# Kernel tuning notes

Hardware: AMD Instinct MI355X
Metric: run time of the kernel (lower is better)

Reference implementation:

```python
import jax, jax.numpy as jnp
import numpy as np

B, N, DIM, H, DH, M = 2, 2048, 1024, 16, 64, 512
INNER = H * DH  # 1024
KV = M + 1 + N  # xl mem + null kv + sequence = 2561


def rotate_half(x):
    x1, x2 = jnp.split(x, 2, axis=-1)
    return jnp.concatenate([-x2, x1], axis=-1)


def apply_rotary_pos_emb(pos, t):
    return t * jnp.cos(pos) + rotate_half(t) * jnp.sin(pos)


def setup_inputs() -> dict:
    key = jax.random.key(0)
    ks = jax.random.split(key, 8)
    return {
        "x": jax.random.normal(ks[0], (B, N, DIM), jnp.float32),
        "rotary_q": jax.random.uniform(ks[1], (N, DH), jnp.float32) * 6.28,
        "rotary_k": jax.random.uniform(ks[2], (KV, DH), jnp.float32) * 6.28,
        "xl_memories": jax.random.normal(ks[3], (2, B, H, M, DH), jnp.float32) * 0.02,
        "Wq": jax.random.normal(ks[4], (DIM, INNER), jnp.float32) * 0.02,
        "Wkv": jax.random.normal(ks[5], (DIM, 2 * INNER), jnp.float32) * 0.02,
        "Wout": jax.random.normal(ks[6], (INNER, INNER), jnp.float32) * 0.02,
        "null_kv": jax.random.normal(ks[7], (2, H, DH), jnp.float32),
    }


def reference(x, rotary_q, rotary_k, xl_memories, Wq, Wkv, Wout, null_kv):
    # QKV projections (no bias, matching keras Dense(use_bias=False))
    q = (x @ Wq).reshape(B, N, H, DH).transpose(0, 2, 1, 3)  # b h n d
    k, v = jnp.split(x @ Wkv, 2, axis=-1)
    k = k.reshape(B, N, H, DH).transpose(0, 2, 1, 3)
    v = v.reshape(B, N, H, DH).transpose(0, 2, 1, 3)

    # prepend learned null key/value (1 token)
    nk = jnp.broadcast_to(null_kv[0][None, :, None, :], (B, H, 1, DH))
    nv = jnp.broadcast_to(null_kv[1][None, :, None, :], (B, H, 1, DH))
    k = jnp.concatenate([nk, k], axis=2)
    v = jnp.concatenate([nv, v], axis=2)

    next_xl_memories = jnp.stack([k, v])  # [2, b, h, 1+n, d]

    # prepend XL memories along key axis
    k = jnp.concatenate([xl_memories[0], k], axis=2)  # b h kv d
    v = jnp.concatenate([xl_memories[1], v], axis=2)

    # inline rotary embedding on q and (full) k
    q = apply_rotary_pos_emb(rotary_q, q)
    k = apply_rotary_pos_emb(rotary_k, k)

    # causal attention with bottom-right aligned mask (mem/null tokens visible)
    scale = DH ** -0.5
    sim = jnp.einsum('bhid,bhjd->bhij', q, k) * scale  # b h n kv
    i = jnp.arange(N)[:, None]
    j = jnp.arange(KV)[None, :]
    causal_ok = j <= (i + (KV - N))
    sim = jnp.where(causal_ok, sim, jnp.finfo(sim.dtype).min)
    attn = jax.nn.softmax(sim, axis=-1)
    out = jnp.einsum('bhij,bhjd->bhid', attn, v)  # b h n d

    out = out.transpose(0, 2, 1, 3).reshape(B, N, INNER)
    return out @ Wout, next_xl_memories
```

## Files before the change

kernel.cpp:

```cpp
#include <hip/hip_runtime.h>


typedef short v8s __attribute__((ext_vector_type(8)));
typedef float v4f __attribute__((ext_vector_type(4)));

__device__ __forceinline__ float bf2f(unsigned short x) {
  return __uint_as_float(((unsigned)x) << 16);
}
__device__ __forceinline__ unsigned short f2bf(float f) {
  unsigned u = __float_as_uint(f);
  u += 0x7FFFu + ((u >> 16) & 1u);
  return (unsigned short)(u >> 16);
}

#if __has_builtin(__builtin_amdgcn_exp2f)
#define EXP2(x) __builtin_amdgcn_exp2f(x)
#else
#define EXP2(x) exp2f(x)
#endif

template <int CTRL>
__device__ __forceinline__ float dppf(float x) {
  return __int_as_float(
      __builtin_amdgcn_update_dpp(0, __float_as_int(x), CTRL, 0xF, 0xF, true));
}
#define DPP_X1 0xB1
#define DPP_X2 0x4E
#define DPP_X7 0x141
#define DPP_XF 0x140

__device__ __forceinline__ float red_sum16(float v) {
  v += dppf<DPP_X1>(v);
  v += dppf<DPP_X2>(v);
  v += dppf<DPP_X7>(v);
  v += dppf<DPP_XF>(v);
  return v;
}

__device__ __forceinline__ void gld_lds16(const void* g, void* l) {
  __builtin_amdgcn_global_load_lds(
      (const __attribute__((address_space(1))) unsigned int*)g,
      (__attribute__((address_space(3))) unsigned int*)l, 16, 0, 0);
}

__global__ __launch_bounds__(256) void cvt_bf16(
    const float* __restrict__ S, unsigned short* __restrict__ D, int n4)
{
  const int i = blockIdx.x * 256 + threadIdx.x;
  if (i < n4) {
    const float4 v = ((const float4*)S)[i];
    ushort4 o;
    o.x = f2bf(v.x); o.y = f2bf(v.y); o.z = f2bf(v.z); o.w = f2bf(v.w);
    ((ushort4*)D)[i] = o;
  }
}

template <typename CT>
__global__ __launch_bounds__(256, 2) void gemm_bf16(
    const unsigned short* __restrict__ A,
    const unsigned short* __restrict__ WT,
    CT* __restrict__ C,
    int K, int ldc)
{
  __shared__ unsigned short As[128 * 64];
  __shared__ unsigned short Bs[128 * 64];
  const int tid  = threadIdx.x;
  const int wave = tid >> 6, lane = tid & 63;
  const int l15  = lane & 15, quad = lane >> 4;
  const int wm   = wave >> 1, wn = wave & 1;
  const int row0 = blockIdx.x * 128, col0 = blockIdx.y * 128;
  const int lrow = lane >> 3;
  const int gsw  = (lane & 7) ^ lrow;

  v4f acc[4][4];
  const v4f vzero = {0.f, 0.f, 0.f, 0.f};
#pragma unroll
  for (int i = 0; i < 4; ++i)
#pragma unroll
    for (int j = 0; j < 4; ++j) acc[i][j] = vzero;

  for (int k0 = 0; k0 < K; k0 += 64) {
    __syncthreads();
#pragma unroll
    for (int ro = 0; ro < 4; ++ro) {
      const int chunk = wave * 4 + ro;
      const int arow  = chunk * 8 + lrow;
      gld_lds16(A  + (size_t)(row0 + arow) * K + k0 + gsw * 8, As + chunk * 512);
      gld_lds16(WT + (size_t)(col0 + arow) * K + k0 + gsw * 8, Bs + chunk * 512);
    }
    __syncthreads();

    v8s af[4][2], bf[4][2];
#pragma unroll
    for (int tm = 0; tm < 4; ++tm) {
      const int r = wm * 64 + tm * 16 + l15;
#pragma unroll
      for (int kk = 0; kk < 2; ++kk) {
        const int slot = (kk * 4 + quad) ^ (r & 7);
        af[tm][kk] = *(const v8s*)(As + r * 64 + slot * 8);
      }
    }
#pragma unroll
    for (int tn = 0; tn < 4; ++tn) {
      const int r = wn * 64 + tn * 16 + l15;
#pragma unroll
      for (int kk = 0; kk < 2; ++kk) {
        const int slot = (kk * 4 + quad) ^ (r & 7);
        bf[tn][kk] = *(const v8s*)(Bs + r * 64 + slot * 8);
      }
    }
#pragma unroll
    for (int kk = 0; kk < 2; ++kk)
#pragma unroll
      for (int tm = 0; tm < 4; ++tm)
#pragma unroll
        for (int tn = 0; tn < 4; ++tn)
          acc[tm][tn] = __builtin_amdgcn_mfma_f32_16x16x32_bf16(
              af[tm][kk], bf[tn][kk], acc[tm][tn], 0, 0, 0);
  }

#pragma unroll
  for (int tm = 0; tm < 4; ++tm)
#pragma unroll
    for (int tn = 0; tn < 4; ++tn)
#pragma unroll
      for (int r = 0; r < 4; ++r) {
        const int row = row0 + wm * 64 + tm * 16 + quad * 4 + r;
        const int col = col0 + wn * 64 + tn * 16 + l15;
        if constexpr (sizeof(CT) == 2)
          C[(size_t)row * ldc + col] = (CT)f2bf(acc[tm][tn][r]);
        else
          C[(size_t)row * ldc + col] = (CT)acc[tm][tn][r];
      }
}

__global__ __launch_bounds__(256) void transpose_wt(
    const float* __restrict__ S0,
    const float* __restrict__ S1,
    int c0, int c1, int K,
    unsigned short* __restrict__ D)
{
  __shared__ float T[64][65];
  const int k0 = blockIdx.x * 64, n0 = blockIdx.y * 64;
  const int tid = threadIdx.x;
#pragma unroll
  for (int ro = 0; ro < 4; ++ro) {
    const int idx = ro * 256 + tid;
    const int kr = idx >> 4, ch = idx & 15;
    const int n = n0 + ch * 4;
    float4 val;
    if (n < c0) val = *(const float4*)(S0 + (size_t)(k0 + kr) * c0 + n);
    else        val = *(const float4*)(S1 + (size_t)(k0 + kr) * c1 + (n - c0));
    T[kr][ch * 4 + 0] = val.x; T[kr][ch * 4 + 1] = val.y;
    T[kr][ch * 4 + 2] = val.z; T[kr][ch * 4 + 3] = val.w;
  }
  __syncthreads();
#pragma unroll
  for (int ro = 0; ro < 2; ++ro) {
    const int idx = ro * 256 + tid;
    const int nl = idx >> 3, ch = idx & 7;
    __align__(16) unsigned short tmp[8];
#pragma unroll
    for (int e = 0; e < 8; ++e) tmp[e] = f2bf(T[ch * 8 + e][nl]);
    *(uint4*)(D + (size_t)(n0 + nl) * K + k0 + ch * 8) = *(const uint4*)tmp;
  }
}

__global__ __launch_bounds__(256) void assemble(
    const unsigned short* __restrict__ QKV,
    const float* __restrict__ rq,
    const float* __restrict__ rk,
    const float* __restrict__ xlm,
    const float* __restrict__ nkv,
    unsigned short* __restrict__ Qrot,
    unsigned short* __restrict__ Kf,
    unsigned short* __restrict__ Vn,
    float* __restrict__ nxl)
{
  const int gw = blockIdx.x * 4 + (threadIdx.x >> 6);
  const int d  = threadIdx.x & 63;
  const int RK = 32 * 2561;
  if (gw < RK) {
    const int bh = gw / 2561;
    const int j  = gw - bh * 2561;
    const int b  = bh >> 4, h = bh & 15;
    float kx, vx;
    if (j < 512) {
      const size_t i0 = (((size_t)(b * 16 + h)) * 512 + j) * 64 + d;
      kx = xlm[i0];
      vx = xlm[1048576 + i0];
    } else if (j == 512) {
      kx = nkv[h * 64 + d];
      vx = nkv[1024 + h * 64 + d];
    } else {
      const size_t rowb = ((size_t)(b * 2048 + (j - 513))) * 3072;
      kx = bf2f(QKV[rowb + 1024 + h * 64 + d]);
      vx = bf2f(QKV[rowb + 2048 + h * 64 + d]);
    }
    Vn[(((size_t)bh) * 2561 + j) * 64 + d] = f2bf(vx);
    if (j >= 512) {
      const size_t o0 = (((size_t)(b * 16 + h)) * 2049 + (j - 512)) * 64 + d;
      nxl[o0] = kx;
      nxl[4196352 + o0] = vx;
    }
    const float ang = rk[j * 64 + d];
    const float cs = __cosf(ang), sn = __sinf(ang);
    const float part = __shfl_xor(kx, 32);
    const float kr = kx * cs + (d < 32 ? -part : part) * sn;
    Kf[(((size_t)bh) * 2624 + j) * 64 + d] = f2bf(kr);
  } else {
    const int g2 = gw - RK;
    const int bh = g2 >> 11, n = g2 & 2047;
    const int b  = bh >> 4, h = bh & 15;
    const float qx = bf2f(QKV[((size_t)(b * 2048 + n)) * 3072 + h * 64 + d]);
    const float ang = rq[n * 64 + d];
    const float cs = __cosf(ang), sn = __sinf(ang);
    const float part = __shfl_xor(qx, 32);
    const float qr = qx * cs + (d < 32 ? -part : part) * sn;
    Qrot[(((size_t)bh) * 2048 + n) * 64 + d] = f2bf(qr * 0.18033688f);
  }
}

__global__ __launch_bounds__(256) void transpose_v(
    const unsigned short* __restrict__ Vn,
    unsigned short* __restrict__ VTp)
{
  __shared__ unsigned short T[64][72];
  const int j0 = blockIdx.x * 64;
  const int bh = blockIdx.y;
  const int tid = threadIdx.x;
#pragma unroll
  for (int ro = 0; ro < 2; ++ro) {
    const int idx = ro * 256 + tid;
    const int jr = idx >> 3, ch = idx & 7;
    uint4 val = make_uint4(0, 0, 0, 0);
    if (j0 + jr < 2561)
      val = *(const uint4*)(Vn + (((size_t)bh) * 2561 + j0 + jr) * 64 + ch * 8);
    *(uint4*)(&T[jr][ch * 8]) = val;
  }
  __syncthreads();
#pragma unroll
  for (int ro = 0; ro < 2; ++ro) {
    const int idx = ro * 256 + tid;
    const int dl = idx >> 3, ch = idx & 7;
    __align__(16) unsigned short tmp[8];
#pragma unroll
    for (int e = 0; e < 8; ++e) tmp[e] = T[ch * 8 + e][dl];
    *(uint4*)(VTp + (((size_t)bh) * 64 + dl) * 2624 + j0 + ch * 8) = *(const uint4*)tmp;
  }
}

__global__ __launch_bounds__(256, 2) void attn_fa(
    const unsigned short* __restrict__ Qr,
    const unsigned short* __restrict__ Kf,
    const unsigned short* __restrict__ VTp,
    unsigned short* __restrict__ Ao)
{
  const int qb = 15 - (int)blockIdx.x;
  const int bh = blockIdx.y;
  const int b = bh >> 4, h = bh & 15;
  __shared__ unsigned short QPs[128 * 72];
  __shared__ unsigned short Ks[64 * 72];
  __shared__ unsigned short Vs[64 * 72];
  const int tid = threadIdx.x;
  const int wave = tid >> 6, lane = tid & 63;
  const int l15 = lane & 15, quad = lane >> 4;
  const v4f vzero = {0.f, 0.f, 0.f, 0.f};

  {
    const unsigned short* Qg = Qr + (((size_t)bh) * 2048 + qb * 128) * 64;
#pragma unroll
    for (int ro = 0; ro < 4; ++ro) {
      const int idx = ro * 256 + tid;
      const int row = idx >> 3, ch = idx & 7;
      *(uint4*)(QPs + row * 72 + ch * 8) = *(const uint4*)(Qg + row * 64 + ch * 8);
    }
  }
  __syncthreads();
  v8s qf[2][2];
#pragma unroll
  for (int mt = 0; mt < 2; ++mt) {
    const int r = mt * 64 + wave * 16 + l15;
    qf[mt][0] = *(const v8s*)(QPs + r * 72 + quad * 8);
    qf[mt][1] = *(const v8s*)(QPs + r * 72 + 32 + quad * 8);
  }
  unsigned short* Pw = QPs + wave * 32 * 72;

  float l_i[2][4] = {{0.f,0.f,0.f,0.f},{0.f,0.f,0.f,0.f}};
  v4f O[2][4];
#pragma unroll
  for (int mt = 0; mt < 2; ++mt)
#pragma unroll
    for (int dt = 0; dt < 4; ++dt) O[mt][dt] = vzero;

  const unsigned short* Kg0 = Kf + (size_t)bh * 2624 * 64;
  const unsigned short* Vg0 = VTp + (size_t)bh * 64 * 2624;
  const int ntiles = (2 * qb + 11 <= 41) ? (2 * qb + 11) : 41;
  const int tfast  = 2 * qb + 7;

  const int srow = tid >> 3, sch = tid & 7;
  const int srow1 = srow + 32;

#define PREFETCH(t, ka, kb, va, vb)                                          \
  {                                                                          \
    const int j0p = (t) * 64;                                                \
    ka = *(const uint4*)(Kg0 + (size_t)(j0p + srow) * 64 + sch * 8);         \
    va = *(const uint4*)(Vg0 + (size_t)srow * 2624 + j0p + sch * 8);         \
    kb = *(const uint4*)(Kg0 + (size_t)(j0p + srow1) * 64 + sch * 8);        \
    vb = *(const uint4*)(Vg0 + (size_t)srow1 * 2624 + j0p + sch * 8);        \
  }
#define STAGE(ka, kb, va, vb)                                                \
  {                                                                          \
    *(uint4*)(Ks + srow * 72 + sch * 8) = ka;                                \
    *(uint4*)(Vs + srow * 72 + sch * 8) = va;                                \
    *(uint4*)(Ks + srow1 * 72 + sch * 8) = kb;                               \
    *(uint4*)(Vs + srow1 * 72 + sch * 8) = vb;                               \
  }

  auto compute_tile = [&](int j0, bool masked) {
    v4f s[2][4];
#pragma unroll
    for (int jt = 0; jt < 4; ++jt) {
      const v8s kfr0 = *(const v8s*)(Ks + (jt * 16 + l15) * 72 + quad * 8);
      const v8s kfr1 = *(const v8s*)(Ks + (jt * 16 + l15) * 72 + 32 + quad * 8);
#pragma unroll
      for (int mt = 0; mt < 2; ++mt) {
        v4f c = vzero;
        c = __builtin_amdgcn_mfma_f32_16x16x32_bf16(qf[mt][0], kfr0, c, 0, 0, 0);
        c = __builtin_amdgcn_mfma_f32_16x16x32_bf16(qf[mt][1], kfr1, c, 0, 0, 0);
        s[mt][jt] = c;
      }
    }

    if (masked) {
#pragma unroll
      for (int mt = 0; mt < 2; ++mt) {
        const int ibase = qb * 128 + mt * 64 + wave * 16 + quad * 4 + 513;
#pragma unroll
        for (int jt = 0; jt < 4; ++jt) {
          const int jg = j0 + jt * 16 + l15;
#pragma unroll
          for (int r = 0; r < 4; ++r)
            s[mt][jt][r] = (jg <= ibase + r) ? s[mt][jt][r] : -1e30f;
        }
      }
    }

#pragma unroll
    for (int mt = 0; mt < 2; ++mt)
#pragma unroll
      for (int r = 0; r < 4; ++r) {
        const float p0 = EXP2(s[mt][0][r]);
        const float p1 = EXP2(s[mt][1][r]);
        const float p2 = EXP2(s[mt][2][r]);
        const float p3 = EXP2(s[mt][3][r]);
        l_i[mt][r] += red_sum16(p0 + p1 + p2 + p3);
        const int prow = (mt * 16 + quad * 4 + r) * 72 + l15;
        Pw[prow]      = f2bf(p0);
        Pw[prow + 16] = f2bf(p1);
        Pw[prow + 32] = f2bf(p2);
        Pw[prow + 48] = f2bf(p3);
      }
    __asm__ volatile("s_waitcnt lgkmcnt(0)" ::: "memory");

    v8s pf[2][2];
#pragma unroll
    for (int mt = 0; mt < 2; ++mt) {
      pf[mt][0] = *(const v8s*)(Pw + (mt * 16 + l15) * 72 + quad * 8);
      pf[mt][1] = *(const v8s*)(Pw + (mt * 16 + l15) * 72 + 32 + quad * 8);
    }
#pragma unroll
    for (int dt = 0; dt < 4; ++dt) {
      const v8s vf0 = *(const v8s*)(Vs + (dt * 16 + l15) * 72 + quad * 8);
      const v8s vf1 = *(const v8s*)(Vs + (dt * 16 + l15) * 72 + 32 + quad * 8);
#pragma unroll
      for (int mt = 0; mt < 2; ++mt) {
        v4f c = O[mt][dt];
        c = __builtin_amdgcn_mfma_f32_16x16x32_bf16(pf[mt][0], vf0, c, 0, 0, 0);
        c = __builtin_amdgcn_mfma_f32_16x16x32_bf16(pf[mt][1], vf1, c, 0, 0, 0);
        O[mt][dt] = c;
      }
    }
  };

  uint4 k0a, k0b, v0a, v0b, k1a, k1b, v1a, v1b;
  PREFETCH(0, k0a, k0b, v0a, v0b);
  for (int t = 0; t < ntiles; t += 2) {
    __syncthreads();
    STAGE(k0a, k0b, v0a, v0b);
    if (t + 1 < ntiles) PREFETCH(t + 1, k1a, k1b, v1a, v1b);
    __syncthreads();
    compute_tile(t * 64, t > tfast);
    if (t + 1 >= ntiles) break;
    __syncthreads();
    STAGE(k1a, k1b, v1a, v1b);
    if (t + 2 < ntiles) PREFETCH(t + 2, k0a, k0b, v0a, v0b);
    __syncthreads();
    compute_tile((t + 1) * 64, (t + 1) > tfast);
  }
#undef PREFETCH
#undef STAGE

#pragma unroll
  for (int mt = 0; mt < 2; ++mt)
#pragma unroll
    for (int r = 0; r < 4; ++r) {
      const float linv = 1.0f / l_i[mt][r];
      const int n = qb * 128 + mt * 64 + wave * 16 + quad * 4 + r;
      const size_t rowbase = ((size_t)b * 2048 + n) * 1024 + h * 64;
#pragma unroll
      for (int dt = 0; dt < 4; ++dt)
        Ao[rowbase + dt * 16 + l15] = f2bf(O[mt][dt][r] * linv);
    }
}

extern "C" void kernel_launch(void* const* d_in, const int* in_sizes, int n_in,
                              void* d_out, int out_size, void* d_ws, size_t ws_size,
                              hipStream_t stream)
{
  const float* x    = (const float*)d_in[0];
  const float* rq   = (const float*)d_in[1];
  const float* rk   = (const float*)d_in[2];
  const float* xlm  = (const float*)d_in[3];
  const float* Wq   = (const float*)d_in[4];
  const float* Wkv  = (const float*)d_in[5];
  const float* Wout = (const float*)d_in[6];
  const float* nkv  = (const float*)d_in[7];
  float* out = (float*)d_out;
  float* nxl = out + 4194304;
  char* ws = (char*)d_ws;
  unsigned short* QKV   = (unsigned short*)(ws + 0);
  unsigned short* xbf   = (unsigned short*)(ws + 25165824);
  unsigned short* Ao    = (unsigned short*)(ws + 25165824);
  unsigned short* WqkvT = (unsigned short*)(ws + 33554432);
  unsigned short* WoutT = (unsigned short*)(ws + 39845888);
  unsigned short* Qrot  = (unsigned short*)(ws + 41943040);
  unsigned short* Kf    = (unsigned short*)(ws + 50331648);
  unsigned short* Vn    = (unsigned short*)(ws + 61079552);
  unsigned short* VTp   = (unsigned short*)(ws + 71569408);

  cvt_bf16<<<4096, 256, 0, stream>>>(x, xbf, 1048576);
  transpose_wt<<<dim3(16, 48), 256, 0, stream>>>(Wq, Wkv, 1024, 2048, 1024, WqkvT);
  transpose_wt<<<dim3(16, 16), 256, 0, stream>>>(Wout, Wout, 1024, 1024, 1024, WoutT);
  gemm_bf16<unsigned short><<<dim3(32, 24), 256, 0, stream>>>(xbf, WqkvT, QKV, 1024, 3072);
  assemble<<<36872, 256, 0, stream>>>(QKV, rq, rk, xlm, nkv, Qrot, Kf, Vn, nxl);
  transpose_v<<<dim3(41, 32), 256, 0, stream>>>(Vn, VTp);
  attn_fa<<<dim3(16, 32), 256, 0, stream>>>(Qrot, Kf, VTp, Ao);
  gemm_bf16<float><<<dim3(32, 8), 256, 0, stream>>>(Ao, WoutT, out, 1024, 1024);
}
```

Measured before the change: 253.4 us.

## Halve attention query tile to 64 rows and stagger block-to-tile mapping

The flash-attention kernel now processes 64 query rows per block instead of 128, with each wave holding one 16-row fragment. This doubles the grid to 1024 blocks and raises the launch-bounds occupancy hint to 4 blocks per CU. The query-block index is rotated by blockIdx.y to interleave long and short causal workloads across the grid. The aim is better load balance and latency hiding, at the cost of loading each K/V tile twice as often per query row, which lowers arithmetic intensity.

```diff
diff --git a/kernel.cpp b/kernel.cpp
--- a/kernel.cpp
+++ b/kernel.cpp
@@ -250,16 +250,16 @@
   }
 }
 
-__global__ __launch_bounds__(256, 2) void attn_fa(
+__global__ __launch_bounds__(256, 4) void attn_fa(
     const unsigned short* __restrict__ Qr,
     const unsigned short* __restrict__ Kf,
     const unsigned short* __restrict__ VTp,
     unsigned short* __restrict__ Ao)
 {
-  const int qb = 15 - (int)blockIdx.x;
   const int bh = blockIdx.y;
+  const int qb = 31 - (int)((blockIdx.x + blockIdx.y) & 31);
   const int b = bh >> 4, h = bh & 15;
-  __shared__ unsigned short QPs[128 * 72];
+  __shared__ unsigned short QPs[64 * 72];
   __shared__ unsigned short Ks[64 * 72];
   __shared__ unsigned short Vs[64 * 72];
   const int tid = threadIdx.x;
@@ -268,35 +268,32 @@
   const v4f vzero = {0.f, 0.f, 0.f, 0.f};
 
   {
-    const unsigned short* Qg = Qr + (((size_t)bh) * 2048 + qb * 128) * 64;
-#pragma unroll
-    for (int ro = 0; ro < 4; ++ro) {
+    const unsigned short* Qg = Qr + (((size_t)bh) * 2048 + qb * 64) * 64;
+#pragma unroll
+    for (int ro = 0; ro < 2; ++ro) {
       const int idx = ro * 256 + tid;
       const int row = idx >> 3, ch = idx & 7;
       *(uint4*)(QPs + row * 72 + ch * 8) = *(const uint4*)(Qg + row * 64 + ch * 8);
     }
   }
   __syncthreads();
-  v8s qf[2][2];
-#pragma unroll
-  for (int mt = 0; mt < 2; ++mt) {
-    const int r = mt * 64 + wave * 16 + l15;
-    qf[mt][0] = *(const v8s*)(QPs + r * 72 + quad * 8);
-    qf[mt][1] = *(const v8s*)(QPs + r * 72 + 32 + quad * 8);
-  }
-  unsigned short* Pw = QPs + wave * 32 * 72;
-
-  float l_i[2][4] = {{0.f,0.f,0.f,0.f},{0.f,0.f,0.f,0.f}};
-  v4f O[2][4];
-#pragma unroll
-  for (int mt = 0; mt < 2; ++mt)
-#pragma unroll
-    for (int dt = 0; dt < 4; ++dt) O[mt][dt] = vzero;
+  v8s qf[2];
+  {
+    const int r = wave * 16 + l15;
+    qf[0] = *(const v8s*)(QPs + r * 72 + quad * 8);
+    qf[1] = *(const v8s*)(QPs + r * 72 + 32 + quad * 8);
+  }
+  unsigned short* Pw = QPs + wave * 16 * 72;
+
+  float l_i[4] = {0.f, 0.f, 0.f, 0.f};
+  v4f O[4];
+#pragma unroll
+  for (int dt = 0; dt < 4; ++dt) O[dt] = vzero;
 
   const unsigned short* Kg0 = Kf + (size_t)bh * 2624 * 64;
   const unsigned short* Vg0 = VTp + (size_t)bh * 64 * 2624;
-  const int ntiles = (2 * qb + 11 <= 41) ? (2 * qb + 11) : 41;
-  const int tfast  = 2 * qb + 7;
+  const int ntiles = (qb + 10 <= 41) ? (qb + 10) : 41;
+  const int tfast  = qb + 7;
 
   const int srow = tid >> 3, sch = tid & 7;
   const int srow1 = srow + 32;
@@ -318,68 +315,54 @@
   }
 
   auto compute_tile = [&](int j0, bool masked) {
-    v4f s[2][4];
+    v4f s[4];
 #pragma unroll
     for (int jt = 0; jt < 4; ++jt) {
       const v8s kfr0 = *(const v8s*)(Ks + (jt * 16 + l15) * 72 + quad * 8);
       const v8s kfr1 = *(const v8s*)(Ks + (jt * 16 + l15) * 72 + 32 + quad * 8);
-#pragma unroll
-      for (int mt = 0; mt < 2; ++mt) {
-        v4f c = vzero;
-        c = __builtin_amdgcn_mfma_f32_16x16x32_bf16(qf[mt][0], kfr0, c, 0, 0, 0);
-        c = __builtin_amdgcn_mfma_f32_16x16x32_bf16(qf[mt][1], kfr1, c, 0, 0, 0);
-        s[mt][jt] = c;
+      v4f c = vzero;
+      c = __builtin_amdgcn_mfma_f32_16x16x32_bf16(qf[0], kfr0, c, 0, 0, 0);
+      c = __builtin_amdgcn_mfma_f32_16x16x32_bf16(qf[1], kfr1, c, 0, 0, 0);
+      s[jt] = c;
+    }
+
+    if (masked) {
+      const int ibase = qb * 64 + wave * 16 + quad * 4 + 513;
+#pragma unroll
+      for (int jt = 0; jt < 4; ++jt) {
+        const int jg = j0 + jt * 16 + l15;
+#pragma unroll
+        for (int r = 0; r < 4; ++r)
+          s[jt][r] = (jg <= ibase + r) ? s[jt][r] : -1e30f;
       }
     }
 
-    if (masked) {
-#pragma unroll
-      for (int mt = 0; mt < 2; ++mt) {
-        const int ibase = qb * 128 + mt * 64 + wave * 16 + quad * 4 + 513;
-#pragma unroll
-        for (int jt = 0; jt < 4; ++jt) {
-          const int jg = j0 + jt * 16 + l15;
-#pragma unroll
-          for (int r = 0; r < 4; ++r)
-            s[mt][jt][r] = (jg <= ibase + r) ? s[mt][jt][r] : -1e30f;
-        }
-      }
-    }
-
-#pragma unroll
-    for (int mt = 0; mt < 2; ++mt)
-#pragma unroll
-      for (int r = 0; r < 4; ++r) {
-        const float p0 = EXP2(s[mt][0][r]);
-        const float p1 = EXP2(s[mt][1][r]);
-        const float p2 = EXP2(s[mt][2][r]);
-        const float p3 = EXP2(s[mt][3][r]);
-        l_i[mt][r] += red_sum16(p0 + p1 + p2 + p3);
-        const int prow = (mt * 16 + quad * 4 + r) * 72 + l15;
-        Pw[prow]      = f2bf(p0);
-        Pw[prow + 16] = f2bf(p1);
-        Pw[prow + 32] = f2bf(p2);
-        Pw[prow + 48] = f2bf(p3);
-      }
+#pragma unroll
+    for (int r = 0; r < 4; ++r) {
+      const float p0 = EXP2(s[0][r]);
+      const float p1 = EXP2(s[1][r]);
+      const float p2 = EXP2(s[2][r]);
+      const float p3 = EXP2(s[3][r]);
+      l_i[r] += red_sum16(p0 + p1 + p2 + p3);
+      const int prow = (quad * 4 + r) * 72 + l15;
+      Pw[prow]      = f2bf(p0);
+      Pw[prow + 16] = f2bf(p1);
+      Pw[prow + 32] = f2bf(p2);
+      Pw[prow + 48] = f2bf(p3);
+    }
     __asm__ volatile("s_waitcnt lgkmcnt(0)" ::: "memory");
 
-    v8s pf[2][2];
-#pragma unroll
-    for (int mt = 0; mt < 2; ++mt) {
-      pf[mt][0] = *(const v8s*)(Pw + (mt * 16 + l15) * 72 + quad * 8);
-      pf[mt][1] = *(const v8s*)(Pw + (mt * 16 + l15) * 72 + 32 + quad * 8);
-    }
+    v8s pf[2];
+    pf[0] = *(const v8s*)(Pw + l15 * 72 + quad * 8);
+    pf[1] = *(const v8s*)(Pw + l15 * 72 + 32 + quad * 8);
 #pragma unroll
     for (int dt = 0; dt < 4; ++dt) {
       const v8s vf0 = *(const v8s*)(Vs + (dt * 16 + l15) * 72 + quad * 8);
       const v8s vf1 = *(const v8s*)(Vs + (dt * 16 + l15) * 72 + 32 + quad * 8);
-#pragma unroll
-      for (int mt = 0; mt < 2; ++mt) {
-        v4f c = O[mt][dt];
-        c = __builtin_amdgcn_mfma_f32_16x16x32_bf16(pf[mt][0], vf0, c, 0, 0, 0);
-        c = __builtin_amdgcn_mfma_f32_16x16x32_bf16(pf[mt][1], vf1, c, 0, 0, 0);
-        O[mt][dt] = c;
-      }
+      v4f c = O[dt];
+      c = __builtin_amdgcn_mfma_f32_16x16x32_bf16(pf[0], vf0, c, 0, 0, 0);
+      c = __builtin_amdgcn_mfma_f32_16x16x32_bf16(pf[1], vf1, c, 0, 0, 0);
+      O[dt] = c;
     }
   };
 
@@ -402,16 +385,14 @@
 #undef STAGE
 
 #pragma unroll
-  for (int mt = 0; mt < 2; ++mt)
-#pragma unroll
-    for (int r = 0; r < 4; ++r) {
-      const float linv = 1.0f / l_i[mt][r];
-      const int n = qb * 128 + mt * 64 + wave * 16 + quad * 4 + r;
-      const size_t rowbase = ((size_t)b * 2048 + n) * 1024 + h * 64;
-#pragma unroll
-      for (int dt = 0; dt < 4; ++dt)
-        Ao[rowbase + dt * 16 + l15] = f2bf(O[mt][dt][r] * linv);
-    }
+  for (int r = 0; r < 4; ++r) {
+    const float linv = 1.0f / l_i[r];
+    const int n = qb * 64 + wave * 16 + quad * 4 + r;
+    const size_t rowbase = ((size_t)b * 2048 + n) * 1024 + h * 64;
+#pragma unroll
+    for (int dt = 0; dt < 4; ++dt)
+      Ao[rowbase + dt * 16 + l15] = f2bf(O[dt][r] * linv);
+  }
 }
 
 extern "C" void kernel_launch(void* const* d_in, const int* in_sizes, int n_in,
@@ -445,6 +426,6 @@
   gemm_bf16<unsigned short><<<dim3(32, 24), 256, 0, stream>>>(xbf, WqkvT, QKV, 1024, 3072);
   assemble<<<36872, 256, 0, stream>>>(QKV, rq, rk, xlm, nkv, Qrot, Kf, Vn, nxl);
   transpose_v<<<dim3(41, 32), 256, 0, stream>>>(Vn, VTp);
-  attn_fa<<<dim3(16, 32), 256, 0, stream>>>(Qrot, Kf, VTp, Ao);
+  attn_fa<<<dim3(32, 32), 256, 0, stream>>>(Qrot, Kf, VTp, Ao);
   gemm_bf16<float><<<dim3(32, 8), 256, 0, stream>>>(Ao, WoutT, out, 1024, 1024);
 }
```

Result: faster. 242.7 us (-4.2%).
